# Kernel optimization log

Measured on AMD Instinct MI355X. Metric: run time of the kernel, lower is better.

Reference implementation:

```python
import jax, jax.numpy as jnp
import numpy as np

NUM_C = 1024
EMB = 512
HID = 512
BATCH = 64
SEQ = 512


def setup_inputs() -> dict:
    key = jax.random.key(0)
    ks = jax.random.split(key, 10)
    q = jax.random.randint(ks[0], (BATCH, SEQ), 0, NUM_C, dtype=jnp.int32)
    r = jax.random.randint(ks[1], (BATCH, SEQ), 0, 2, dtype=jnp.int32)
    s = 1.0 / np.sqrt(HID)
    emb = jax.random.normal(ks[2], (NUM_C * 2, EMB), dtype=jnp.float32)
    Wh_w = jax.random.uniform(ks[3], (HID, HID), jnp.float32, -s, s)
    Wh_b = jax.random.uniform(ks[4], (HID,), jnp.float32, -s, s)
    Wx_w = jax.random.uniform(ks[5], (HID, EMB), jnp.float32, -s, s)
    Wx_b = jax.random.uniform(ks[6], (HID,), jnp.float32, -s, s)
    tau = jnp.ones((HID,), jnp.float32)
    Wo_w = jax.random.uniform(ks[7], (NUM_C, HID), jnp.float32, -s, s)
    Wo_b = jax.random.uniform(ks[8], (NUM_C,), jnp.float32, -s, s)
    return {"q": q, "r": r, "emb": emb, "Wh_w": Wh_w, "Wh_b": Wh_b,
            "Wx_w": Wx_w, "Wx_b": Wx_b, "tau": tau, "Wo_w": Wo_w, "Wo_b": Wo_b}


def reference(q, r, emb, Wh_w, Wh_b, Wx_w, Wx_b, tau, Wo_w, Wo_b):
    # interaction embedding: x = q + num_c * r
    idx = q + NUM_C * r                      # [B, S]
    xemb = emb[idx]                          # [B, S, E]
    # precompute input projection for all timesteps (faithful: same sum)
    xproj = jnp.einsum('bse,he->bsh', xemb, Wx_w) + Wx_b + Wh_b  # [B, S, H]

    def step(h, xp_t):
        # liquid time-constant cell update
        dh = (-h + jnp.tanh(h @ Wh_w.T + xp_t)) / tau
        h_new = h + dh
        return h_new, h_new

    h0 = jnp.zeros((q.shape[0], HID), xemb.dtype)
    _, hs = jax.lax.scan(step, h0, jnp.swapaxes(xproj, 0, 1))  # hs: [S, B, H]
    outputs = jnp.swapaxes(hs, 0, 1)         # [B, S, H]
    # dropout is identity at inference
    y = jax.nn.sigmoid(jnp.einsum('bsh,ch->bsc', outputs, Wo_w) + Wo_b)
    return y
```

## Files before the change

kernel.cpp:

```cpp
#include <hip/hip_runtime.h>
#include <hip/hip_bf16.h>

#define NUM_C 1024
#define EMB   512
#define HID   512
#define BATCH 64
#define SEQ   512

typedef short bf16x8 __attribute__((ext_vector_type(8)));
typedef float f32x4  __attribute__((ext_vector_type(4)));

__device__ __forceinline__ unsigned short f2bf(float x) {
    unsigned u = __float_as_uint(x);
    u += 0x7fffu + ((u >> 16) & 1u);
    return (unsigned short)(u >> 16);
}
__device__ __forceinline__ unsigned pack2bf(float a, float b) {
    return (unsigned)f2bf(a) | ((unsigned)f2bf(b) << 16);
}
__device__ __forceinline__ float uaf(unsigned u) { return __uint_as_float(u); }

__device__ __forceinline__ float ftanh(float x) {
    float e = __expf(2.f * x);
    return 1.f - 2.f / (e + 1.f);
}

__global__ __launch_bounds__(256) void f32_to_bf16(const float* __restrict__ src,
                                                   unsigned short* __restrict__ dst, int n) {
    int i = blockIdx.x * 256 + threadIdx.x;
    if (i < n) dst[i] = f2bf(src[i]);
}

__global__ __launch_bounds__(256)
void gemm_nt_f32(const float* __restrict__ A, const float* __restrict__ B,
                 float* __restrict__ C, int M, int N, int K,
                 const float* __restrict__ bias1, const float* __restrict__ bias2) {
    __shared__ float As[64][33];
    __shared__ float Bs[64][33];

    const int n0 = blockIdx.x * 64;
    const int m0 = blockIdx.y * 64;
    const int tid = threadIdx.x;
    const int tx = tid & 15;
    const int ty = tid >> 4;

    float acc[4][4] = {{0.f}};

    for (int k0 = 0; k0 < K; k0 += 32) {
        #pragma unroll
        for (int i = 0; i < 2; ++i) {
            int f   = tid * 2 + i;
            int row = f >> 3;
            int kf  = f & 7;
            float4 va = *(const float4*)&A[(size_t)(m0 + row) * K + k0 + kf * 4];
            float4 vb = *(const float4*)&B[(size_t)(n0 + row) * K + k0 + kf * 4];
            As[row][kf * 4 + 0] = va.x; As[row][kf * 4 + 1] = va.y;
            As[row][kf * 4 + 2] = va.z; As[row][kf * 4 + 3] = va.w;
            Bs[row][kf * 4 + 0] = vb.x; Bs[row][kf * 4 + 1] = vb.y;
            Bs[row][kf * 4 + 2] = vb.z; Bs[row][kf * 4 + 3] = vb.w;
        }
        __syncthreads();
        #pragma unroll
        for (int kk = 0; kk < 32; ++kk) {
            float a[4], b[4];
            #pragma unroll
            for (int i = 0; i < 4; ++i) a[i] = As[ty * 4 + i][kk];
            #pragma unroll
            for (int j = 0; j < 4; ++j) b[j] = Bs[tx * 4 + j][kk];
            #pragma unroll
            for (int i = 0; i < 4; ++i)
                #pragma unroll
                for (int j = 0; j < 4; ++j)
                    acc[i][j] += a[i] * b[j];
        }
        __syncthreads();
    }

    float bb[4];
    #pragma unroll
    for (int j = 0; j < 4; ++j) {
        int n = n0 + tx * 4 + j;
        bb[j] = bias1[n] + bias2[n];
    }
    #pragma unroll
    for (int i = 0; i < 4; ++i) {
        size_t m = (size_t)(m0 + ty * 4 + i);
        float4 ov;
        ov.x = acc[i][0] + bb[0]; ov.y = acc[i][1] + bb[1];
        ov.z = acc[i][2] + bb[2]; ov.w = acc[i][3] + bb[3];
        *(float4*)&C[m * N + n0 + tx * 4] = ov;
    }
}

__global__ __launch_bounds__(512, 2)
void ltc_scan15(const int* __restrict__ q, const int* __restrict__ r,
                const float* __restrict__ emb_proj, const float* __restrict__ Wh,
                const float* __restrict__ tau, float* __restrict__ hx) {
    __shared__ float hfA[512], hfB[512];
    __shared__ float psA[512], psB[512];
    __shared__ int   idA[512], idB[512];

    const int tid  = threadIdx.x;
    const int sl   = blockIdx.x >> 5;
    const int bp   = blockIdx.x & 31;
    const int bA   = bp * 2, bB = bA + 1;
    const int lane = tid & 63;
    const int w    = tid >> 6;

    float4 wr_[16];
    {
        const float* wrow = Wh + (size_t)(sl * 64 + lane) * 512 + w * 64;
        #pragma unroll
        for (int i = 0; i < 16; ++i) wr_[i] = ((const float4*)wrow)[i];
    }

    hfA[tid] = 0.f; hfB[tid] = 0.f;
    psA[tid] = 0.f;
    idA[tid] = q[bA * SEQ + tid] + NUM_C * r[bA * SEQ + tid];
    idB[tid] = q[bB * SEQ + tid] + NUM_C * r[bB * SEQ + tid];

    const bool fin = (w == sl);
    float rtau = 0.f, hA = 0.f, hB = 0.f, eA = 0.f, eB = 0.f;
    if (fin) rtau = 1.0f / tau[sl * 64 + lane];

    float* hxA = hx + (size_t)bA * SEQ * HID;
    float* hxB = hx + (size_t)bB * SEQ * HID;
    const float4* hA4 = (const float4*)(hfA + w * 64);
    const float4* hB4 = (const float4*)(hfB + w * 64);
    __syncthreads();

    if (fin) {
        eA = emb_proj[(size_t)idA[0] * HID + sl * 64 + lane];
        eB = emb_proj[(size_t)idB[0] * HID + sl * 64 + lane];
    }

    for (int s = 0; s < SEQ; ++s) {
        if (fin) {
            float pre = eA;
            #pragma unroll
            for (int m = 0; m < 8; ++m) pre += psA[m * 64 + lane];
            float hn = hA + (ftanh(pre) - hA) * rtau;
            hA = hn;
            __hip_atomic_store((unsigned*)&hxA[s * 512 + sl * 64 + lane],
                               __float_as_uint(hn), __ATOMIC_RELAXED,
                               __HIP_MEMORY_SCOPE_AGENT);
            hfA[sl * 64 + lane] = hn;
            if (s + 1 < SEQ)
                eA = emb_proj[(size_t)idA[s + 1] * HID + sl * 64 + lane];
        } else if (s > 0) {
            unsigned* ap = (unsigned*)&hxB[(s - 1) * 512 + w * 64 + lane];
            unsigned wi = __hip_atomic_load(ap, __ATOMIC_RELAXED,
                                            __HIP_MEMORY_SCOPE_AGENT);
            while ((wi & 0x7f800000u) == 0x7f800000u) {
                __builtin_amdgcn_s_sleep(1);
                wi = __hip_atomic_load(ap, __ATOMIC_RELAXED,
                                       __HIP_MEMORY_SCOPE_AGENT);
            }
            hfB[w * 64 + lane] = uaf(wi);
        }
        {
            float a0 = 0.f, a1 = 0.f, a2 = 0.f, a3 = 0.f;
            #pragma unroll
            for (int i = 0; i < 16; ++i) {
                float4 hv = hB4[i];
                a0 = fmaf(wr_[i].x, hv.x, a0);
                a1 = fmaf(wr_[i].y, hv.y, a1);
                a2 = fmaf(wr_[i].z, hv.z, a2);
                a3 = fmaf(wr_[i].w, hv.w, a3);
            }
            psB[w * 64 + lane] = (a0 + a1) + (a2 + a3);
        }
        __syncthreads();

        if (fin) {
            float pre = eB;
            #pragma unroll
            for (int m = 0; m < 8; ++m) pre += psB[m * 64 + lane];
            float hn = hB + (ftanh(pre) - hB) * rtau;
            hB = hn;
            __hip_atomic_store((unsigned*)&hxB[s * 512 + sl * 64 + lane],
                               __float_as_uint(hn), __ATOMIC_RELAXED,
                               __HIP_MEMORY_SCOPE_AGENT);
            hfB[sl * 64 + lane] = hn;
            if (s + 1 < SEQ)
                eB = emb_proj[(size_t)idB[s + 1] * HID + sl * 64 + lane];
        } else if (s + 1 < SEQ) {
            unsigned* ap = (unsigned*)&hxA[s * 512 + w * 64 + lane];
            unsigned wi = __hip_atomic_load(ap, __ATOMIC_RELAXED,
                                            __HIP_MEMORY_SCOPE_AGENT);
            while ((wi & 0x7f800000u) == 0x7f800000u) {
                __builtin_amdgcn_s_sleep(1);
                wi = __hip_atomic_load(ap, __ATOMIC_RELAXED,
                                       __HIP_MEMORY_SCOPE_AGENT);
            }
            hfA[w * 64 + lane] = uaf(wi);
        }
        if (s + 1 < SEQ) {
            float a0 = 0.f, a1 = 0.f, a2 = 0.f, a3 = 0.f;
            #pragma unroll
            for (int i = 0; i < 16; ++i) {
                float4 hv = hA4[i];
                a0 = fmaf(wr_[i].x, hv.x, a0);
                a1 = fmaf(wr_[i].y, hv.y, a1);
                a2 = fmaf(wr_[i].z, hv.z, a2);
                a3 = fmaf(wr_[i].w, hv.w, a3);
            }
            psA[w * 64 + lane] = (a0 + a1) + (a2 + a3);
        }
        __syncthreads();
    }
}

__global__ __launch_bounds__(256)
void gemm_out_bf16(const float* __restrict__ A,
                   const unsigned short* __restrict__ B,
                   const float* __restrict__ bias,
                   float* __restrict__ C, int M) {
    __shared__ __align__(16) unsigned short As[128 * 32];
    __shared__ __align__(16) unsigned short Bs[128 * 32];

    const int tid = threadIdx.x;
    const int n0 = blockIdx.x * 128;
    const int m0 = blockIdx.y * 128;
    const int w  = tid >> 6;
    const int l  = tid & 63;
    const int wr = w >> 1, wc = w & 1;
    const int lr = l & 15;
    const int lq = l >> 4;

    f32x4 acc[4][4];
    #pragma unroll
    for (int i = 0; i < 4; ++i)
        #pragma unroll
        for (int jn = 0; jn < 4; ++jn)
            acc[i][jn] = (f32x4){0.f, 0.f, 0.f, 0.f};

    for (int k0 = 0; k0 < 512; k0 += 32) {
        #pragma unroll
        for (int p = 0; p < 2; ++p) {
            int flat = p * 256 + tid;
            int row  = flat >> 2;
            int c4   = flat & 3;
            const float* asrc = &A[(size_t)(m0 + row) * 512 + k0 + c4 * 8];
            float4 v0 = ((const float4*)asrc)[0];
            float4 v1 = ((const float4*)asrc)[1];
            uint4 d;
            d.x = pack2bf(v0.x, v0.y); d.y = pack2bf(v0.z, v0.w);
            d.z = pack2bf(v1.x, v1.y); d.w = pack2bf(v1.z, v1.w);
            *(uint4*)&As[row * 32 + c4 * 8] = d;
            *(uint4*)&Bs[row * 32 + c4 * 8] =
                *(const uint4*)&B[(size_t)(n0 + row) * 512 + k0 + c4 * 8];
        }
        __syncthreads();

        bf16x8 af[4], bf[4];
        #pragma unroll
        for (int mf = 0; mf < 4; ++mf)
            af[mf] = *(const bf16x8*)&As[(wr * 64 + mf * 16 + lr) * 32 + lq * 8];
        #pragma unroll
        for (int nf = 0; nf < 4; ++nf)
            bf[nf] = *(const bf16x8*)&Bs[(wc * 64 + nf * 16 + lr) * 32 + lq * 8];

        #pragma unroll
        for (int mf = 0; mf < 4; ++mf)
            #pragma unroll
            for (int nf = 0; nf < 4; ++nf)
                acc[mf][nf] = __builtin_amdgcn_mfma_f32_16x16x32_bf16(
                    af[mf], bf[nf], acc[mf][nf], 0, 0, 0);
        __syncthreads();
    }

    #pragma unroll
    for (int mf = 0; mf < 4; ++mf) {
        #pragma unroll
        for (int nf = 0; nf < 4; ++nf) {
            int col = n0 + wc * 64 + nf * 16 + lr;
            float bb = bias[col];
            #pragma unroll
            for (int reg = 0; reg < 4; ++reg) {
                int rowm = m0 + wr * 64 + mf * 16 + lq * 4 + reg;
                float v = acc[mf][nf][reg] + bb;
                C[(size_t)rowm * 1024 + col] = 1.0f / (1.0f + expf(-v));
            }
        }
    }
}

extern "C" void kernel_launch(void* const* d_in, const int* in_sizes, int n_in,
                              void* d_out, int out_size, void* d_ws, size_t ws_size,
                              hipStream_t stream) {
    const int*   q    = (const int*)d_in[0];
    const int*   r    = (const int*)d_in[1];
    const float* emb  = (const float*)d_in[2];
    const float* Wh_w = (const float*)d_in[3];
    const float* Wh_b = (const float*)d_in[4];
    const float* Wx_w = (const float*)d_in[5];
    const float* Wx_b = (const float*)d_in[6];
    const float* tau  = (const float*)d_in[7];
    const float* Wo_w = (const float*)d_in[8];
    const float* Wo_b = (const float*)d_in[9];
    float* out = (float*)d_out;

    char* ws = (char*)d_ws;
    float*          emb_proj = (float*)ws;
    unsigned short* Wobf     = (unsigned short*)(ws + (4u << 20));
    float*          hx       = (float*)(ws + (5u << 20));

    hipMemsetAsync(hx, 0xFF, (size_t)BATCH * SEQ * HID * 4, stream);

    f32_to_bf16<<<(1024 * 512) / 256, 256, 0, stream>>>(Wo_w, Wobf, 1024 * 512);

    gemm_nt_f32<<<dim3(512 / 64, 2048 / 64), 256, 0, stream>>>(
        emb, Wx_w, emb_proj, 2048, 512, 512, Wx_b, Wh_b);

    ltc_scan15<<<256, 512, 0, stream>>>(q, r, emb_proj, Wh_w, tau, hx);

    gemm_out_bf16<<<dim3(1024 / 128, (BATCH * SEQ) / 128), 256, 0, stream>>>(
        hx, Wobf, Wo_b, out, BATCH * SEQ);
}
```

Before: 943.2 us.

## Broadcast hidden state via readlane and issue spin loads before dot products

```diff
diff --git a/kernel.cpp b/kernel.cpp
--- a/kernel.cpp
+++ b/kernel.cpp
@@ -93,10 +93,9 @@
 }
 
 __global__ __launch_bounds__(512, 2)
-void ltc_scan15(const int* __restrict__ q, const int* __restrict__ r,
+void ltc_scan18(const int* __restrict__ q, const int* __restrict__ r,
                 const float* __restrict__ emb_proj, const float* __restrict__ Wh,
                 const float* __restrict__ tau, float* __restrict__ hx) {
-    __shared__ float hfA[512], hfB[512];
     __shared__ float psA[512], psB[512];
     __shared__ int   idA[512], idB[512];
 
@@ -114,19 +113,17 @@
         for (int i = 0; i < 16; ++i) wr_[i] = ((const float4*)wrow)[i];
     }
 
-    hfA[tid] = 0.f; hfB[tid] = 0.f;
-    psA[tid] = 0.f;
     idA[tid] = q[bA * SEQ + tid] + NUM_C * r[bA * SEQ + tid];
     idB[tid] = q[bB * SEQ + tid] + NUM_C * r[bB * SEQ + tid];
+    psA[tid] = 0.f;
 
     const bool fin = (w == sl);
     float rtau = 0.f, hA = 0.f, hB = 0.f, eA = 0.f, eB = 0.f;
+    int wiA = 0, wiB = 0;
     if (fin) rtau = 1.0f / tau[sl * 64 + lane];
 
-    float* hxA = hx + (size_t)bA * SEQ * HID;
-    float* hxB = hx + (size_t)bB * SEQ * HID;
-    const float4* hA4 = (const float4*)(hfA + w * 64);
-    const float4* hB4 = (const float4*)(hfB + w * 64);
+    unsigned* hxAw = (unsigned*)(hx + (size_t)bA * SEQ * HID);
+    unsigned* hxBw = (unsigned*)(hx + (size_t)bB * SEQ * HID);
     __syncthreads();
 
     if (fin) {
@@ -135,79 +132,98 @@
     }
 
     for (int s = 0; s < SEQ; ++s) {
+        unsigned ldB = 0;
+        if (!fin && s > 0)
+            ldB = __hip_atomic_load(&hxBw[(s - 1) * 512 + w * 64 + lane],
+                                    __ATOMIC_RELAXED, __HIP_MEMORY_SCOPE_AGENT);
+        if (fin && s > 0) {
+            float pre = eB;
+            #pragma unroll
+            for (int m = 0; m < 8; ++m) pre += psB[m * 64 + lane];
+            float hn = hB + (ftanh(pre) - hB) * rtau;
+            hB = hn;
+            __hip_atomic_store(&hxBw[(s - 1) * 512 + sl * 64 + lane],
+                               __float_as_uint(hn), __ATOMIC_RELAXED,
+                               __HIP_MEMORY_SCOPE_AGENT);
+            wiB = (int)__float_as_uint(hn);
+            eB = emb_proj[(size_t)idB[s] * HID + sl * 64 + lane];
+        }
+        {
+            float a0 = 0.f, a1 = 0.f, a2 = 0.f, a3 = 0.f;
+            #pragma unroll
+            for (int i = 0; i < 16; ++i) {
+                a0 = fmaf(wr_[i].x,
+                     uaf((unsigned)__builtin_amdgcn_readlane(wiA, 4 * i + 0)), a0);
+                a1 = fmaf(wr_[i].y,
+                     uaf((unsigned)__builtin_amdgcn_readlane(wiA, 4 * i + 1)), a1);
+                a2 = fmaf(wr_[i].z,
+                     uaf((unsigned)__builtin_amdgcn_readlane(wiA, 4 * i + 2)), a2);
+                a3 = fmaf(wr_[i].w,
+                     uaf((unsigned)__builtin_amdgcn_readlane(wiA, 4 * i + 3)), a3);
+            }
+            psA[w * 64 + lane] = (a0 + a1) + (a2 + a3);
+        }
+        if (!fin && s > 0) {
+            while ((ldB & 0x7f800000u) == 0x7f800000u) {
+                __builtin_amdgcn_s_sleep(1);
+                ldB = __hip_atomic_load(&hxBw[(s - 1) * 512 + w * 64 + lane],
+                                        __ATOMIC_RELAXED, __HIP_MEMORY_SCOPE_AGENT);
+            }
+            wiB = (int)ldB;
+        }
+        __syncthreads();
+
+        unsigned ldA = 0;
+        if (!fin)
+            ldA = __hip_atomic_load(&hxAw[s * 512 + w * 64 + lane],
+                                    __ATOMIC_RELAXED, __HIP_MEMORY_SCOPE_AGENT);
         if (fin) {
             float pre = eA;
             #pragma unroll
             for (int m = 0; m < 8; ++m) pre += psA[m * 64 + lane];
             float hn = hA + (ftanh(pre) - hA) * rtau;
             hA = hn;
-            __hip_atomic_store((unsigned*)&hxA[s * 512 + sl * 64 + lane],
+            __hip_atomic_store(&hxAw[s * 512 + sl * 64 + lane],
                                __float_as_uint(hn), __ATOMIC_RELAXED,
                                __HIP_MEMORY_SCOPE_AGENT);
-            hfA[sl * 64 + lane] = hn;
+            wiA = (int)__float_as_uint(hn);
             if (s + 1 < SEQ)
                 eA = emb_proj[(size_t)idA[s + 1] * HID + sl * 64 + lane];
-        } else if (s > 0) {
-            unsigned* ap = (unsigned*)&hxB[(s - 1) * 512 + w * 64 + lane];
-            unsigned wi = __hip_atomic_load(ap, __ATOMIC_RELAXED,
-                                            __HIP_MEMORY_SCOPE_AGENT);
-            while ((wi & 0x7f800000u) == 0x7f800000u) {
-                __builtin_amdgcn_s_sleep(1);
-                wi = __hip_atomic_load(ap, __ATOMIC_RELAXED,
-                                       __HIP_MEMORY_SCOPE_AGENT);
-            }
-            hfB[w * 64 + lane] = uaf(wi);
         }
         {
             float a0 = 0.f, a1 = 0.f, a2 = 0.f, a3 = 0.f;
             #pragma unroll
             for (int i = 0; i < 16; ++i) {
-                float4 hv = hB4[i];
-                a0 = fmaf(wr_[i].x, hv.x, a0);
-                a1 = fmaf(wr_[i].y, hv.y, a1);
-                a2 = fmaf(wr_[i].z, hv.z, a2);
-                a3 = fmaf(wr_[i].w, hv.w, a3);
+                a0 = fmaf(wr_[i].x,
+                     uaf((unsigned)__builtin_amdgcn_readlane(wiB, 4 * i + 0)), a0);
+                a1 = fmaf(wr_[i].y,
+                     uaf((unsigned)__builtin_amdgcn_readlane(wiB, 4 * i + 1)), a1);
+                a2 = fmaf(wr_[i].z,
+                     uaf((unsigned)__builtin_amdgcn_readlane(wiB, 4 * i + 2)), a2);
+                a3 = fmaf(wr_[i].w,
+                     uaf((unsigned)__builtin_amdgcn_readlane(wiB, 4 * i + 3)), a3);
             }
             psB[w * 64 + lane] = (a0 + a1) + (a2 + a3);
         }
-        __syncthreads();
-
-        if (fin) {
-            float pre = eB;
-            #pragma unroll
-            for (int m = 0; m < 8; ++m) pre += psB[m * 64 + lane];
-            float hn = hB + (ftanh(pre) - hB) * rtau;
-            hB = hn;
-            __hip_atomic_store((unsigned*)&hxB[s * 512 + sl * 64 + lane],
-                               __float_as_uint(hn), __ATOMIC_RELAXED,
-                               __HIP_MEMORY_SCOPE_AGENT);
-            hfB[sl * 64 + lane] = hn;
-            if (s + 1 < SEQ)
-                eB = emb_proj[(size_t)idB[s + 1] * HID + sl * 64 + lane];
-        } else if (s + 1 < SEQ) {
-            unsigned* ap = (unsigned*)&hxA[s * 512 + w * 64 + lane];
-            unsigned wi = __hip_atomic_load(ap, __ATOMIC_RELAXED,
-                                            __HIP_MEMORY_SCOPE_AGENT);
-            while ((wi & 0x7f800000u) == 0x7f800000u) {
+        if (!fin) {
+            while ((ldA & 0x7f800000u) == 0x7f800000u) {
                 __builtin_amdgcn_s_sleep(1);
-                wi = __hip_atomic_load(ap, __ATOMIC_RELAXED,
-                                       __HIP_MEMORY_SCOPE_AGENT);
-            }
-            hfA[w * 64 + lane] = uaf(wi);
-        }
-        if (s + 1 < SEQ) {
-            float a0 = 0.f, a1 = 0.f, a2 = 0.f, a3 = 0.f;
-            #pragma unroll
-            for (int i = 0; i < 16; ++i) {
-                float4 hv = hA4[i];
-                a0 = fmaf(wr_[i].x, hv.x, a0);
-                a1 = fmaf(wr_[i].y, hv.y, a1);
-                a2 = fmaf(wr_[i].z, hv.z, a2);
-                a3 = fmaf(wr_[i].w, hv.w, a3);
-            }
-            psA[w * 64 + lane] = (a0 + a1) + (a2 + a3);
-        }
-        __syncthreads();
+                ldA = __hip_atomic_load(&hxAw[s * 512 + w * 64 + lane],
+                                        __ATOMIC_RELAXED, __HIP_MEMORY_SCOPE_AGENT);
+            }
+            wiA = (int)ldA;
+        }
+        __syncthreads();
+    }
+
+    if (fin) {
+        float pre = eB;
+        #pragma unroll
+        for (int m = 0; m < 8; ++m) pre += psB[m * 64 + lane];
+        float hn = hB + (ftanh(pre) - hB) * rtau;
+        __hip_atomic_store(&hxBw[(SEQ - 1) * 512 + sl * 64 + lane],
+                           __float_as_uint(hn), __ATOMIC_RELAXED,
+                           __HIP_MEMORY_SCOPE_AGENT);
     }
 }
 
@@ -313,7 +329,7 @@
     gemm_nt_f32<<<dim3(512 / 64, 2048 / 64), 256, 0, stream>>>(
         emb, Wx_w, emb_proj, 2048, 512, 512, Wx_b, Wh_b);
 
-    ltc_scan15<<<256, 512, 0, stream>>>(q, r, emb_proj, Wh_w, tau, hx);
+    ltc_scan18<<<256, 512, 0, stream>>>(q, r, emb_proj, Wh_w, tau, hx);
 
     gemm_out_bf16<<<dim3(1024 / 128, (BATCH * SEQ) / 128), 256, 0, stream>>>(
         hx, Wobf, Wo_b, out, BATCH * SEQ);
```

After: 910.6 us. 1.04x faster.
